# Performance work log

Measured on AMD Instinct MI355X. Metric: run time of the kernel, lower is better.

## Reference

```python
import jax, jax.numpy as jnp
import numpy as np

N, E, B, EP = 100000, 1600000, 512, 200000
NIN, NEMB, HID, NL = 64, 64, 72, 3
EPS = 1e-5


def setup_inputs() -> dict:
    key = jax.random.key(0)
    ks = jax.random.split(key, 20)
    inp = {
        'x': jax.random.normal(ks[0], (N, NIN), jnp.float32),
        'emb': jax.random.normal(ks[1], (N, NEMB), jnp.float32),
        'assign': jax.random.uniform(ks[2], (N, B), jnp.float32),
        'edge_index': jax.random.randint(ks[3], (2, E), 0, N, jnp.int64),
        'pedge_index': jax.random.randint(ks[4], (2, EP), 0, B, jnp.int64),
        # params (xavier-ish scale)
        'node_w': jax.random.normal(ks[5], (NIN, HID), jnp.float32) / np.sqrt(NIN),
        'node_b': jnp.zeros((HID,), jnp.float32),
        'emb_w': jax.random.normal(ks[6], (NEMB, HID), jnp.float32) / np.sqrt(NEMB),
        'emb_b': jnp.zeros((HID,), jnp.float32),
        'conv_winit': jax.random.normal(ks[7], (NL, HID, HID), jnp.float32) / np.sqrt(HID),
        'conv_wroot': jax.random.normal(ks[8], (NL, HID, HID), jnp.float32) / np.sqrt(HID),
        'conv_bias': jnp.zeros((NL, HID), jnp.float32),
        'bn_gamma': jnp.ones((NL, HID), jnp.float32),
        'bn_beta': jnp.zeros((NL, HID), jnp.float32),
        'mlp_w1': jax.random.normal(ks[9], (12 * HID, HID), jnp.float32) / np.sqrt(12 * HID),
        'mlp_b1': jnp.zeros((HID,), jnp.float32),
        'mlp_w2': jax.random.normal(ks[10], (HID, 1), jnp.float32) / np.sqrt(HID),
        'mlp_b2': jnp.zeros((1,), jnp.float32),
    }
    return inp


def _forward(x, emb, assign, node_w, node_b, emb_w, emb_b, conv_winit,
             conv_wroot, conv_bias, bn_gamma, bn_beta, mlp_w1, mlp_b1,
             mlp_w2, mlp_b2, edge_index, pedge_index):
    n = x.shape[0]
    nb = assign.shape[1]
    row, col = edge_index[0], edge_index[1]
    # gcn_norm without self-loops (ARMAConv): D^{-1/2} A D^{-1/2}
    deg = jax.ops.segment_sum(jnp.ones((row.shape[0],), x.dtype), col, num_segments=n)
    dis = jnp.where(deg > 0, jax.lax.rsqrt(jnp.maximum(deg, 1.0)) * jnp.where(deg > 0, 1.0, 0.0), 0.0)
    dis = jnp.where(deg > 0, deg ** -0.5, 0.0)
    norm = dis[row] * dis[col]

    h = jax.nn.relu(x @ node_w + node_b)  # [N, HID]
    for l in range(NL):
        # ARMAConv K=1, T=1: relu(A_hat (h Wi) + h Wr + b)
        m = norm[:, None] * (h @ conv_winit[l])[row]        # [E, HID]
        agg = jax.ops.segment_sum(m, col, num_segments=n)   # [N, HID]
        h = jax.nn.relu(agg + h @ conv_wroot[l] + conv_bias[l])
        # F.relu applied again in forward (idempotent), then BatchNorm (training stats)
        mu = h.mean(0)
        var = ((h - mu) ** 2).mean(0)
        h = (h - mu) * jax.lax.rsqrt(var + EPS) * bn_gamma[l] + bn_beta[l]

    e = jax.nn.relu(emb @ emb_w + emb_b)
    z = jnp.concatenate([h, e], axis=-1)  # [N, 2*HID]

    batch = jnp.argmax(assign, axis=-1)
    cnt = jax.ops.segment_sum(jnp.ones((n,), z.dtype), batch, num_segments=nb)
    p1 = jax.ops.segment_sum(z, batch, num_segments=nb)
    p2 = jax.ops.segment_max(z, batch, num_segments=nb)
    p3 = p1 / jnp.maximum(cnt, 1.0)[:, None]
    xp = jnp.concatenate([p1, p2, p3], axis=-1)  # [B, 6*HID]

    pair = jnp.concatenate([xp[pedge_index[0]], xp[pedge_index[1]]], axis=1)  # [EP, 12*HID]
    out = jnp.tanh(pair @ mlp_w1 + mlp_b1) @ mlp_w2 + mlp_b2
    return out


def reference(x, emb, assign, edge_index, pedge_index, node_w, node_b, emb_w,
              emb_b, conv_winit, conv_wroot, conv_bias, bn_gamma, bn_beta,
              mlp_w1, mlp_b1, mlp_w2, mlp_b2):
    return _forward(x, emb, assign, node_w, node_b, emb_w, emb_b, conv_winit,
                    conv_wroot, conv_bias, bn_gamma, bn_beta, mlp_w1, mlp_b1,
                    mlp_w2, mlp_b2, edge_index, pedge_index)
```

## Files before the change

### kernel.cpp

```cpp
#include <hip/hip_runtime.h>
#include <hip/hip_bf16.h>

#define HID 72
#define EPSV 1e-5f
#define CAP 64
#define DP 76
#define GF 128
#define GA 2048

__device__ __forceinline__ float tanh_fast(float x) {
    float cx = fminf(fmaxf(x, -15.f), 15.f);
    float e = __expf(2.f * cx);
    return __fdividef(e - 1.f, e + 1.f);
}
__device__ __forceinline__ void fma4(float4& a, float w, const float4 v) {
    a.x += w * v.x; a.y += w * v.y; a.z += w * v.z; a.w += w * v.w;
}

__global__ void k_init(int* deg, float* stats, int* bcnt, int N, int statlen, int B) {
    int i = blockIdx.x * blockDim.x + threadIdx.x;
    if (i < N) deg[i] = 0;
    if (i < statlen) stats[i] = 0.f;
    if (i < B) bcnt[i] = 0;
}

__global__ __launch_bounds__(256) void k_front(const int* __restrict__ row, const int* __restrict__ col,
                                               int* __restrict__ deg, int* __restrict__ csr_r, int E,
                                               const float* __restrict__ x, const float* __restrict__ node_w,
                                               const float* __restrict__ node_b, float* __restrict__ t_buf,
                                               const float* __restrict__ emb, const float* __restrict__ emb_w,
                                               const float* __restrict__ emb_b, float* __restrict__ e_buf,
                                               const float* __restrict__ assign, int* __restrict__ batchv,
                                               int* __restrict__ bcnt, int N, int B, int GD) {
    __shared__ float ws[HID][DP];
    int tid = threadIdx.x;
    int bid = blockIdx.x;

    if (bid < GF) {
        int stride = GF * 256 * 8;
        for (int base = (bid * 256 + tid) * 8; base < E; base += stride) {
            #pragma unroll
            for (int h = 0; h < 2; h++) {
                int eb = base + h * 4;
                if (eb + 3 < E) {
                    int4 cc = *(const int4*)(col + eb);
                    int4 rr = *(const int4*)(row + eb);
                    int p0 = atomicAdd(&deg[cc.x], 1);
                    int p1 = atomicAdd(&deg[cc.y], 1);
                    int p2 = atomicAdd(&deg[cc.z], 1);
                    int p3 = atomicAdd(&deg[cc.w], 1);
                    if (p0 < CAP) csr_r[(size_t)cc.x * CAP + p0] = rr.x;
                    if (p1 < CAP) csr_r[(size_t)cc.y * CAP + p1] = rr.y;
                    if (p2 < CAP) csr_r[(size_t)cc.z * CAP + p2] = rr.z;
                    if (p3 < CAP) csr_r[(size_t)cc.w * CAP + p3] = rr.w;
                } else if (eb < E) {
                    int lim = (eb + 4 < E) ? eb + 4 : E;
                    for (int e = eb; e < lim; e++) {
                        int c = col[e];
                        int pos = atomicAdd(&deg[c], 1);
                        if (pos < CAP) csr_r[(size_t)c * CAP + pos] = row[e];
                    }
                }
            }
        }
        return;
    }
    bid -= GF;
    if (bid < 2 * GD) {
        const float* xin; const float* W; const float* bias; float* out;
        int tb = bid;
        if (tb < GD) { xin = x;   W = node_w; bias = node_b; out = t_buf; }
        else         { xin = emb; W = emb_w;  bias = emb_b;  out = e_buf; tb -= GD; }
        int n0 = tb * 128;
        for (int i = tid; i < 64 * HID; i += 256) {
            int k = i / HID, f = i % HID;
            ws[f][k] = W[i];
        }
        __syncthreads();
        int tn = tid & 31;
        int tf = (tid >> 5) * 9;
        float acc[4][9];
        #pragma unroll
        for (int j = 0; j < 9; j++) {
            float b = bias[tf + j];
            acc[0][j] = b; acc[1][j] = b; acc[2][j] = b; acc[3][j] = b;
        }
        int g0 = n0 + tn;
        const float4* xp0 = (const float4*)(xin + (size_t)(g0      < N ? g0      : N - 1) * 64);
        const float4* xp1 = (const float4*)(xin + (size_t)(g0 + 32 < N ? g0 + 32 : N - 1) * 64);
        const float4* xp2 = (const float4*)(xin + (size_t)(g0 + 64 < N ? g0 + 64 : N - 1) * 64);
        const float4* xp3 = (const float4*)(xin + (size_t)(g0 + 96 < N ? g0 + 96 : N - 1) * 64);
        #pragma unroll 2
        for (int k4 = 0; k4 < 16; k4++) {
            float4 h0 = xp0[k4];
            float4 h1 = xp1[k4];
            float4 h2 = xp2[k4];
            float4 h3 = xp3[k4];
            int k = k4 * 4;
            #pragma unroll
            for (int j = 0; j < 9; j++) {
                float4 w = *(const float4*)&ws[tf + j][k];
                acc[0][j] += h0.x * w.x + h0.y * w.y + h0.z * w.z + h0.w * w.w;
                acc[1][j] += h1.x * w.x + h1.y * w.y + h1.z * w.z + h1.w * w.w;
                acc[2][j] += h2.x * w.x + h2.y * w.y + h2.z * w.z + h2.w * w.w;
                acc[3][j] += h3.x * w.x + h3.y * w.y + h3.z * w.z + h3.w * w.w;
            }
        }
        #pragma unroll
        for (int i = 0; i < 4; i++) {
            int gn = n0 + tn + 32 * i;
            if (gn >= N) continue;
            float* dst = out + (size_t)gn * HID + tf;
            #pragma unroll
            for (int j = 0; j < 9; j++) dst[j] = fmaxf(acc[i][j], 0.f);
        }
        return;
    }
    bid -= 2 * GD;
    int wib = tid >> 6;
    int lane = tid & 63;
    int nq = B / 4;
    for (int n = bid * 4 + wib; n < N; n += GA * 4) {
        const float4* rp4 = (const float4*)(assign + (size_t)n * B);
        float best = -INFINITY;
        int bidx = 0x7fffffff;
        for (int q = lane; q < nq; q += 64) {
            float4 v = rp4[q];
            int j = q * 4;
            if (v.x > best) { best = v.x; bidx = j; }
            if (v.y > best) { best = v.y; bidx = j + 1; }
            if (v.z > best) { best = v.z; bidx = j + 2; }
            if (v.w > best) { best = v.w; bidx = j + 3; }
        }
        #pragma unroll
        for (int off = 32; off > 0; off >>= 1) {
            float ov = __shfl_down(best, off);
            int oi = __shfl_down(bidx, off);
            if (ov > best || (ov == best && oi < bidx)) { best = ov; bidx = oi; }
        }
        if (lane == 0) {
            batchv[n] = bidx;
            atomicAdd(&bcnt[bidx], 1);
        }
    }
}

#define CP 76
template <bool BN, bool DIS>
__global__ __launch_bounds__(256) void k_conv_t(const float* t, const float* __restrict__ stats,
                                                const float* __restrict__ gamma, const float* __restrict__ beta,
                                                const float* __restrict__ wi, const float* __restrict__ wr,
                                                const float* __restrict__ cb, float* __restrict__ hw,
                                                float* agg, int N, float invN,
                                                const int* __restrict__ deg, float* __restrict__ dis) {
    __shared__ float hs[64][CP];
    __shared__ float ws[2 * HID][CP];
    int tid = threadIdx.x;
    int n0 = blockIdx.x * 64;
    if constexpr (DIS) {
        if (tid < 64) {
            int gn = n0 + tid;
            if (gn < N) {
                int d = deg[gn];
                dis[gn] = (d > 0) ? rsqrtf((float)d) : 0.f;
            }
        }
    }
    for (int i = tid; i < HID * 2 * HID; i += 256) {
        int k = i / (2 * HID), f = i % (2 * HID);
        ws[f][k] = (f < HID) ? wi[k * HID + f] : wr[k * HID + (f - HID)];
    }
    for (int i = tid; i < 64 * HID; i += 256) {
        int n = i / HID, f = i % HID;
        int gn = n0 + n;
        float v = (gn < N) ? t[(size_t)gn * HID + f] : 0.f;
        if constexpr (BN) {
            float mu = stats[f] * invN;
            float var = stats[HID + f] * invN - mu * mu;
            v = (v - mu) * rsqrtf(var + EPSV) * gamma[f] + beta[f];
        }
        hs[n][f] = v;
    }
    __syncthreads();
    int tn = tid & 15;
    int tf = (tid >> 4) * 9;
    float acc[4][9];
    #pragma unroll
    for (int j = 0; j < 9; j++) {
        float b = (tf >= HID) ? cb[tf - HID + j] : 0.f;
        acc[0][j] = b; acc[1][j] = b; acc[2][j] = b; acc[3][j] = b;
    }
    #pragma unroll 2
    for (int k4 = 0; k4 < HID / 4; k4++) {
        int k = k4 * 4;
        float4 h0 = *(const float4*)&hs[tn][k];
        float4 h1 = *(const float4*)&hs[tn + 16][k];
        float4 h2 = *(const float4*)&hs[tn + 32][k];
        float4 h3 = *(const float4*)&hs[tn + 48][k];
        #pragma unroll
        for (int j = 0; j < 9; j++) {
            float4 w = *(const float4*)&ws[tf + j][k];
            acc[0][j] += h0.x * w.x + h0.y * w.y + h0.z * w.z + h0.w * w.w;
            acc[1][j] += h1.x * w.x + h1.y * w.y + h1.z * w.z + h1.w * w.w;
            acc[2][j] += h2.x * w.x + h2.y * w.y + h2.z * w.z + h2.w * w.w;
            acc[3][j] += h3.x * w.x + h3.y * w.y + h3.z * w.z + h3.w * w.w;
        }
    }
    #pragma unroll
    for (int i = 0; i < 4; i++) {
        int gn = n0 + tn + 16 * i;
        if (gn >= N) continue;
        float* dst = (tf < HID) ? (hw + (size_t)gn * HID + tf) : (agg + (size_t)gn * HID + (tf - HID));
        #pragma unroll
        for (int j = 0; j < 9; j++) dst[j] = acc[i][j];
    }
}

__global__ __launch_bounds__(256) void k_gather9(const float* __restrict__ hw, const int* __restrict__ deg,
                                                 const int* __restrict__ csr_r, const float* __restrict__ dis,
                                                 float* t, int N) {
    int tid = blockIdx.x * blockDim.x + threadIdx.x;
    int n = tid / 9;
    int s = tid - n * 9;
    if (n >= N) return;
    float4* trow = (float4*)(t + (size_t)n * HID) + s * 2;
    float4 a0 = trow[0], a1 = trow[1];
    int d = deg[n];
    d = (d > CAP) ? CAP : d;
    float disc = dis[n];
    const int* crow = csr_r + (size_t)n * CAP;
    const float4* hb = (const float4*)hw + s * 2;
    for (int j0 = 0; j0 < d; j0 += 4) {
        int4 rr = *(const int4*)(crow + j0);
        int rem = d - j0;
        {
            float w = disc * dis[rr.x];
            const float4* hp = hb + (size_t)rr.x * 18;
            fma4(a0, w, hp[0]); fma4(a1, w, hp[1]);
        }
        if (rem > 1) {
            float w = disc * dis[rr.y];
            const float4* hp = hb + (size_t)rr.y * 18;
            fma4(a0, w, hp[0]); fma4(a1, w, hp[1]);
        }
        if (rem > 2) {
            float w = disc * dis[rr.z];
            const float4* hp = hb + (size_t)rr.z * 18;
            fma4(a0, w, hp[0]); fma4(a1, w, hp[1]);
        }
        if (rem > 3) {
            float w = disc * dis[rr.w];
            const float4* hp = hb + (size_t)rr.w * 18;
            fma4(a0, w, hp[0]); fma4(a1, w, hp[1]);
        }
    }
    trow[0] = make_float4(fmaxf(a0.x, 0.f), fmaxf(a0.y, 0.f), fmaxf(a0.z, 0.f), fmaxf(a0.w, 0.f));
    trow[1] = make_float4(fmaxf(a1.x, 0.f), fmaxf(a1.y, 0.f), fmaxf(a1.z, 0.f), fmaxf(a1.w, 0.f));
}

__global__ __launch_bounds__(256) void k_stats(const float* __restrict__ t, float* __restrict__ st, int total4) {
    __shared__ float s1[HID], s2[HID];
    int tx = threadIdx.x;
    if (tx < HID) s1[tx] = 0.f;
    else if (tx < 2 * HID) s2[tx - HID] = 0.f;
    __syncthreads();
    int stride = gridDim.x * blockDim.x;
    int i0 = blockIdx.x * blockDim.x + tx;
    int f0 = (i0 * 4) % HID;
    float a0 = 0, a1 = 0, a2 = 0, a3 = 0, q0 = 0, q1 = 0, q2 = 0, q3 = 0;
    const float4* tp = (const float4*)t;
    for (int i = i0; i < total4; i += stride) {
        float4 v = tp[i];
        a0 += v.x; q0 += v.x * v.x;
        a1 += v.y; q1 += v.y * v.y;
        a2 += v.z; q2 += v.z * v.z;
        a3 += v.w; q3 += v.w * v.w;
    }
    atomicAdd(&s1[f0 + 0], a0); atomicAdd(&s2[f0 + 0], q0);
    atomicAdd(&s1[f0 + 1], a1); atomicAdd(&s2[f0 + 1], q1);
    atomicAdd(&s1[f0 + 2], a2); atomicAdd(&s2[f0 + 2], q2);
    atomicAdd(&s1[f0 + 3], a3); atomicAdd(&s2[f0 + 3], q3);
    __syncthreads();
    if (tx < HID) {
        atomicAdd(&st[tx], s1[tx]);
        atomicAdd(&st[HID + tx], s2[tx]);
    }
}

__global__ __launch_bounds__(1024) void k_bscan(const int* __restrict__ bcnt, int* __restrict__ boffs,
                                                int* __restrict__ bcur, int B) {
    __shared__ int lds[1024];
    int t = threadIdx.x;
    int v = (t < B) ? bcnt[t] : 0;
    lds[t] = v;
    __syncthreads();
    for (int off = 1; off < 1024; off <<= 1) {
        int x = (t >= off) ? lds[t - off] : 0;
        __syncthreads();
        lds[t] += x;
        __syncthreads();
    }
    if (t < B) {
        int excl = lds[t] - v;
        boffs[t] = excl;
        bcur[t] = excl;
    }
}

__global__ void k_bfill(const int* __restrict__ batchv, int* __restrict__ bcur, int* __restrict__ nlist, int N) {
    int n = blockIdx.x * blockDim.x + threadIdx.x;
    if (n < N) {
        int b = batchv[n];
        int pos = atomicAdd(&bcur[b], 1);
        nlist[pos] = n;
    }
}

__global__ __launch_bounds__(576) void k_poolB(const float* __restrict__ t2, const float* __restrict__ ebuf,
                                               const float* __restrict__ stats2, const float* __restrict__ g2,
                                               const float* __restrict__ bt2, const int* __restrict__ boffs,
                                               const int* __restrict__ bcnt, const int* __restrict__ nlist,
                                               float* __restrict__ xp, float invN) {
    __shared__ float ls[4][2 * HID], lm[4][2 * HID];
    int b = blockIdx.x;
    int tid = threadIdx.x;
    int f = tid % (2 * HID);
    int ch = tid / (2 * HID);
    bool isH = f < HID;
    float a = 1.f, sh = 0.f;
    const float* src;
    if (isH) {
        float s1v = stats2[f], s2v = stats2[HID + f];
        float mu = s1v * invN;
        float var = s2v * invN - mu * mu;
        float inv = rsqrtf(var + EPSV);
        a = inv * g2[f];
        sh = bt2[f] - mu * a;
        src = t2 + f;
    } else {
        src = ebuf + (f - HID);
    }
    int s = boffs[b];
    int c = bcnt[b];
    int e = s + c;
    float sum = 0.f, mx = -INFINITY;
    for (int i = s + ch; i < e; i += 4) {
        float v = src[(size_t)nlist[i] * HID] * a + sh;
        sum += v;
        mx = fmaxf(mx, v);
    }
    ls[ch][f] = sum;
    lm[ch][f] = mx;
    __syncthreads();
    if (ch == 0) {
        float stot = ls[0][f] + ls[1][f] + ls[2][f] + ls[3][f];
        float mtot = fmaxf(fmaxf(lm[0][f], lm[1][f]), fmaxf(lm[2][f], lm[3][f]));
        float* xr = xp + (size_t)b * (6 * HID);
        xr[f] = stot;
        xr[2 * HID + f] = mtot;
        xr[4 * HID + f] = stot / fmaxf((float)c, 1.f);
    }
}

__global__ __launch_bounds__(192) void k_uv(const float* __restrict__ xp, const float* __restrict__ w1,
                                            const float* __restrict__ b1, float* __restrict__ U,
                                            float* __restrict__ V) {
    int b = blockIdx.x;
    int t = threadIdx.x;
    if (t >= 2 * HID) return;
    int half = t / HID;
    int f = t % HID;
    const float* xr = xp + (size_t)b * (6 * HID);
    const float* wb = w1 + (size_t)half * (6 * HID) * HID + f;
    float acc = (half == 0) ? b1[f] : 0.f;
    #pragma unroll 4
    for (int k = 0; k < 6 * HID; k++) acc += xr[k] * wb[(size_t)k * HID];
    if (half == 0) U[(size_t)b * HID + f] = acc;
    else           V[(size_t)b * HID + f] = acc;
}

__global__ __launch_bounds__(256) void k_edge(const int* __restrict__ pe, const float* __restrict__ U,
                                              const float* __restrict__ V, const float* __restrict__ w2,
                                              const float* __restrict__ b2, float* __restrict__ out, int EP) {
    int ep = blockIdx.x * blockDim.x + threadIdx.x;
    if (ep >= EP) return;
    int a = pe[ep];
    int b = pe[EP + ep];
    const float4* up = (const float4*)(U + (size_t)a * HID);
    const float4* vp = (const float4*)(V + (size_t)b * HID);
    float s = 0.f;
    #pragma unroll
    for (int q = 0; q < HID / 4; q++) {
        float4 u = up[q];
        float4 v = vp[q];
        s += tanh_fast(u.x + v.x) * w2[q * 4 + 0];
        s += tanh_fast(u.y + v.y) * w2[q * 4 + 1];
        s += tanh_fast(u.z + v.z) * w2[q * 4 + 2];
        s += tanh_fast(u.w + v.w) * w2[q * 4 + 3];
    }
    out[ep] = s + b2[0];
}

extern "C" void kernel_launch(void* const* d_in, const int* in_sizes, int n_in,
                              void* d_out, int out_size, void* d_ws, size_t ws_size,
                              hipStream_t stream) {
    const float* x       = (const float*)d_in[0];
    const float* emb     = (const float*)d_in[1];
    const float* assign  = (const float*)d_in[2];
    const int*   ei      = (const int*)d_in[3];
    const int*   pe      = (const int*)d_in[4];
    const float* node_w  = (const float*)d_in[5];
    const float* node_b  = (const float*)d_in[6];
    const float* emb_w   = (const float*)d_in[7];
    const float* emb_b   = (const float*)d_in[8];
    const float* conv_wi = (const float*)d_in[9];
    const float* conv_wr = (const float*)d_in[10];
    const float* conv_b  = (const float*)d_in[11];
    const float* bn_g    = (const float*)d_in[12];
    const float* bn_b    = (const float*)d_in[13];
    const float* w1      = (const float*)d_in[14];
    const float* b1      = (const float*)d_in[15];
    const float* w2      = (const float*)d_in[16];
    const float* b2      = (const float*)d_in[17];

    int N = in_sizes[0] / 64;
    int B = in_sizes[2] / N;
    int E = in_sizes[3] / 2;
    int EP = in_sizes[4] / 2;
    float invN = 1.0f / (float)N;

    char* wp = (char*)d_ws;
    auto alloc = [&](size_t nbytes) -> void* {
        void* p = (void*)wp;
        wp += (nbytes + 255) & ~(size_t)255;
        return p;
    };
    float* t_buf  = (float*)alloc((size_t)N * HID * 4);
    float* hw     = (float*)alloc((size_t)N * HID * 4);
    float* e_buf  = (float*)alloc((size_t)N * HID * 4);
    int*   csr_r  = (int*)alloc((size_t)N * CAP * 4);
    int*   deg    = (int*)alloc((size_t)N * 4);
    float* dis    = (float*)alloc((size_t)N * 4);
    int*   batchv = (int*)alloc((size_t)N * 4);
    int*   nlist  = (int*)alloc((size_t)N * 4);
    float* stats  = (float*)alloc((size_t)3 * 2 * HID * 4);
    int*   bcnt   = (int*)alloc((size_t)B * 4);
    int*   boffs  = (int*)alloc((size_t)B * 4);
    int*   bcur   = (int*)alloc((size_t)B * 4);
    float* xp     = (float*)alloc((size_t)B * 6 * HID * 4);
    float* Ub     = (float*)alloc((size_t)B * HID * 4);
    float* Vb     = (float*)alloc((size_t)B * HID * 4);

    const int* row = ei;
    const int* col = ei + E;

    int nb256_N = (N + 255) / 256;
    int GD = (N + 127) / 128;

    k_init<<<nb256_N, 256, 0, stream>>>(deg, stats, bcnt, N, 3 * 2 * HID, B);

    k_front<<<GF + 2 * GD + GA, 256, 0, stream>>>(row, col, deg, csr_r, E,
                                                  x, node_w, node_b, t_buf,
                                                  emb, emb_w, emb_b, e_buf,
                                                  assign, batchv, bcnt, N, B, GD);

    for (int l = 0; l < 3; l++) {
        const float* wi = conv_wi + (size_t)l * HID * HID;
        const float* wr = conv_wr + (size_t)l * HID * HID;
        const float* cb = conv_b + (size_t)l * HID;
        if (l == 0)
            k_conv_t<false, true><<<(N + 63) / 64, 256, 0, stream>>>(t_buf, nullptr, nullptr, nullptr,
                                                                     wi, wr, cb, hw, t_buf, N, invN,
                                                                     deg, dis);
        else
            k_conv_t<true, false><<<(N + 63) / 64, 256, 0, stream>>>(t_buf, stats + (size_t)(l - 1) * 2 * HID,
                                                                     bn_g + (size_t)(l - 1) * HID,
                                                                     bn_b + (size_t)(l - 1) * HID,
                                                                     wi, wr, cb, hw, t_buf, N, invN,
                                                                     nullptr, nullptr);
        k_gather9<<<(9 * N + 255) / 256, 256, 0, stream>>>(hw, deg, csr_r, dis, t_buf, N);
        k_stats<<<288, 256, 0, stream>>>(t_buf, stats + (size_t)l * 2 * HID, N * HID / 4);
    }

    k_bscan<<<1, 1024, 0, stream>>>(bcnt, boffs, bcur, B);
    k_bfill<<<nb256_N, 256, 0, stream>>>(batchv, bcur, nlist, N);
    k_poolB<<<B, 576, 0, stream>>>(t_buf, e_buf, stats + (size_t)2 * 2 * HID,
                                   bn_g + (size_t)2 * HID, bn_b + (size_t)2 * HID,
                                   boffs, bcnt, nlist, xp, invN);
    k_uv<<<B, 192, 0, stream>>>(xp, w1, b1, Ub, Vb);
    k_edge<<<(EP + 255) / 256, 256, 0, stream>>>(pe, Ub, Vb, w2, b2, (float*)d_out, EP);
}
```

Before: 1.235 ms.

## Fuse init, node GEMM, layer-0 conv, and batch scan/fill into fewer launches

Result: no change. 1.227 ms (-0.6%).

```diff
diff --git a/kernel.cpp b/kernel.cpp
--- a/kernel.cpp
+++ b/kernel.cpp
@@ -5,7 +5,7 @@
 #define EPSV 1e-5f
 #define CAP 64
 #define DP 76
-#define GF 128
+#define GF 384
 #define GA 2048
 
 __device__ __forceinline__ float tanh_fast(float x) {
@@ -16,23 +16,79 @@
 __device__ __forceinline__ void fma4(float4& a, float w, const float4 v) {
     a.x += w * v.x; a.y += w * v.y; a.z += w * v.z; a.w += w * v.w;
 }
-
-__global__ void k_init(int* deg, float* stats, int* bcnt, int N, int statlen, int B) {
-    int i = blockIdx.x * blockDim.x + threadIdx.x;
-    if (i < N) deg[i] = 0;
-    if (i < statlen) stats[i] = 0.f;
-    if (i < B) bcnt[i] = 0;
-}
-
-__global__ __launch_bounds__(256) void k_front(const int* __restrict__ row, const int* __restrict__ col,
-                                               int* __restrict__ deg, int* __restrict__ csr_r, int E,
-                                               const float* __restrict__ x, const float* __restrict__ node_w,
-                                               const float* __restrict__ node_b, float* __restrict__ t_buf,
-                                               const float* __restrict__ emb, const float* __restrict__ emb_w,
-                                               const float* __restrict__ emb_b, float* __restrict__ e_buf,
-                                               const float* __restrict__ assign, int* __restrict__ batchv,
-                                               int* __restrict__ bcnt, int N, int B, int GD) {
+__device__ __forceinline__ float inv_sqrt_deg(int d) {
+    return (d > 0) ? rsqrtf((float)d) : 0.f;
+}
+
+__global__ __launch_bounds__(256) void k_d1(const float* __restrict__ x, const float* __restrict__ node_w,
+                                            const float* __restrict__ node_b, float* __restrict__ t_buf,
+                                            int* __restrict__ deg, float* __restrict__ stats,
+                                            int* __restrict__ bcnt, int N, int B, int GD) {
     __shared__ float ws[HID][DP];
+    int tid = threadIdx.x;
+    int bid = blockIdx.x;
+    if (bid >= GD) {
+        int j = (bid - GD) * 256 + tid;
+        if (j < N) deg[j] = 0;
+        if (j < 3 * 2 * HID) stats[j] = 0.f;
+        if (j < B) bcnt[j] = 0;
+        return;
+    }
+    int n0 = bid * 128;
+    for (int i = tid; i < 64 * HID; i += 256) {
+        int k = i / HID, f = i % HID;
+        ws[f][k] = node_w[i];
+    }
+    __syncthreads();
+    int tn = tid & 31;
+    int tf = (tid >> 5) * 9;
+    float acc[4][9];
+    #pragma unroll
+    for (int j = 0; j < 9; j++) {
+        float b = node_b[tf + j];
+        acc[0][j] = b; acc[1][j] = b; acc[2][j] = b; acc[3][j] = b;
+    }
+    int g0 = n0 + tn;
+    const float4* xp0 = (const float4*)(x + (size_t)(g0      < N ? g0      : N - 1) * 64);
+    const float4* xp1 = (const float4*)(x + (size_t)(g0 + 32 < N ? g0 + 32 : N - 1) * 64);
+    const float4* xp2 = (const float4*)(x + (size_t)(g0 + 64 < N ? g0 + 64 : N - 1) * 64);
+    const float4* xp3 = (const float4*)(x + (size_t)(g0 + 96 < N ? g0 + 96 : N - 1) * 64);
+    #pragma unroll 2
+    for (int k4 = 0; k4 < 16; k4++) {
+        float4 h0 = xp0[k4];
+        float4 h1 = xp1[k4];
+        float4 h2 = xp2[k4];
+        float4 h3 = xp3[k4];
+        int k = k4 * 4;
+        #pragma unroll
+        for (int j = 0; j < 9; j++) {
+            float4 w = *(const float4*)&ws[tf + j][k];
+            acc[0][j] += h0.x * w.x + h0.y * w.y + h0.z * w.z + h0.w * w.w;
+            acc[1][j] += h1.x * w.x + h1.y * w.y + h1.z * w.z + h1.w * w.w;
+            acc[2][j] += h2.x * w.x + h2.y * w.y + h2.z * w.z + h2.w * w.w;
+            acc[3][j] += h3.x * w.x + h3.y * w.y + h3.z * w.z + h3.w * w.w;
+        }
+    }
+    #pragma unroll
+    for (int i = 0; i < 4; i++) {
+        int gn = n0 + tn + 32 * i;
+        if (gn >= N) continue;
+        float* dst = t_buf + (size_t)gn * HID + tf;
+        #pragma unroll
+        for (int j = 0; j < 9; j++) dst[j] = fmaxf(acc[i][j], 0.f);
+    }
+}
+
+__global__ __launch_bounds__(256) void k_front2(const int* __restrict__ row, const int* __restrict__ col,
+                                                int* __restrict__ deg, int* __restrict__ csr_r, int E,
+                                                const float* __restrict__ wi0, const float* __restrict__ wr0,
+                                                const float* __restrict__ cb0, float* __restrict__ t_buf,
+                                                float* __restrict__ hw,
+                                                const float* __restrict__ emb, const float* __restrict__ emb_w,
+                                                const float* __restrict__ emb_b, float* __restrict__ e_buf,
+                                                const float* __restrict__ assign, int* __restrict__ batchv,
+                                                int* __restrict__ bcnt, int N, int B, int GDE, int GC) {
+    __shared__ float ws2[2 * HID][DP];
     int tid = threadIdx.x;
     int bid = blockIdx.x;
 
@@ -66,15 +122,59 @@
         return;
     }
     bid -= GF;
-    if (bid < 2 * GD) {
-        const float* xin; const float* W; const float* bias; float* out;
-        int tb = bid;
-        if (tb < GD) { xin = x;   W = node_w; bias = node_b; out = t_buf; }
-        else         { xin = emb; W = emb_w;  bias = emb_b;  out = e_buf; tb -= GD; }
-        int n0 = tb * 128;
+    if (bid < GC) {
+        int n0 = bid * 64;
+        for (int i = tid; i < HID * 2 * HID; i += 256) {
+            int k = i / (2 * HID), f = i % (2 * HID);
+            ws2[f][k] = (f < HID) ? wi0[k * HID + f] : wr0[k * HID + (f - HID)];
+        }
+        __syncthreads();
+        int tn = tid & 15;
+        int tf = (tid >> 4) * 9;
+        float acc[4][9];
+        #pragma unroll
+        for (int j = 0; j < 9; j++) {
+            float b = (tf >= HID) ? cb0[tf - HID + j] : 0.f;
+            acc[0][j] = b; acc[1][j] = b; acc[2][j] = b; acc[3][j] = b;
+        }
+        int g0 = n0 + tn;
+        const float* r0 = t_buf + (size_t)(g0      < N ? g0      : N - 1) * HID;
+        const float* r1 = t_buf + (size_t)(g0 + 16 < N ? g0 + 16 : N - 1) * HID;
+        const float* r2 = t_buf + (size_t)(g0 + 32 < N ? g0 + 32 : N - 1) * HID;
+        const float* r3 = t_buf + (size_t)(g0 + 48 < N ? g0 + 48 : N - 1) * HID;
+        #pragma unroll 2
+        for (int k4 = 0; k4 < HID / 4; k4++) {
+            int k = k4 * 4;
+            float4 h0 = *(const float4*)(r0 + k);
+            float4 h1 = *(const float4*)(r1 + k);
+            float4 h2 = *(const float4*)(r2 + k);
+            float4 h3 = *(const float4*)(r3 + k);
+            #pragma unroll
+            for (int j = 0; j < 9; j++) {
+                float4 w = *(const float4*)&ws2[tf + j][k];
+                acc[0][j] += h0.x * w.x + h0.y * w.y + h0.z * w.z + h0.w * w.w;
+                acc[1][j] += h1.x * w.x + h1.y * w.y + h1.z * w.z + h1.w * w.w;
+                acc[2][j] += h2.x * w.x + h2.y * w.y + h2.z * w.z + h2.w * w.w;
+                acc[3][j] += h3.x * w.x + h3.y * w.y + h3.z * w.z + h3.w * w.w;
+            }
+        }
+        __syncthreads();
+        #pragma unroll
+        for (int i = 0; i < 4; i++) {
+            int gn = n0 + tn + 16 * i;
+            if (gn >= N) continue;
+            float* dst = (tf < HID) ? (hw + (size_t)gn * HID + tf) : (t_buf + (size_t)gn * HID + (tf - HID));
+            #pragma unroll
+            for (int j = 0; j < 9; j++) dst[j] = acc[i][j];
+        }
+        return;
+    }
+    bid -= GC;
+    if (bid < GDE) {
+        int n0 = bid * 128;
         for (int i = tid; i < 64 * HID; i += 256) {
             int k = i / HID, f = i % HID;
-            ws[f][k] = W[i];
+            ws2[f][k] = emb_w[i];
         }
         __syncthreads();
         int tn = tid & 31;
@@ -82,14 +182,14 @@
         float acc[4][9];
         #pragma unroll
         for (int j = 0; j < 9; j++) {
-            float b = bias[tf + j];
+            float b = emb_b[tf + j];
             acc[0][j] = b; acc[1][j] = b; acc[2][j] = b; acc[3][j] = b;
         }
         int g0 = n0 + tn;
-        const float4* xp0 = (const float4*)(xin + (size_t)(g0      < N ? g0      : N - 1) * 64);
-        const float4* xp1 = (const float4*)(xin + (size_t)(g0 + 32 < N ? g0 + 32 : N - 1) * 64);
-        const float4* xp2 = (const float4*)(xin + (size_t)(g0 + 64 < N ? g0 + 64 : N - 1) * 64);
-        const float4* xp3 = (const float4*)(xin + (size_t)(g0 + 96 < N ? g0 + 96 : N - 1) * 64);
+        const float4* xp0 = (const float4*)(emb + (size_t)(g0      < N ? g0      : N - 1) * 64);
+        const float4* xp1 = (const float4*)(emb + (size_t)(g0 + 32 < N ? g0 + 32 : N - 1) * 64);
+        const float4* xp2 = (const float4*)(emb + (size_t)(g0 + 64 < N ? g0 + 64 : N - 1) * 64);
+        const float4* xp3 = (const float4*)(emb + (size_t)(g0 + 96 < N ? g0 + 96 : N - 1) * 64);
         #pragma unroll 2
         for (int k4 = 0; k4 < 16; k4++) {
             float4 h0 = xp0[k4];
@@ -99,7 +199,7 @@
             int k = k4 * 4;
             #pragma unroll
             for (int j = 0; j < 9; j++) {
-                float4 w = *(const float4*)&ws[tf + j][k];
+                float4 w = *(const float4*)&ws2[tf + j][k];
                 acc[0][j] += h0.x * w.x + h0.y * w.y + h0.z * w.z + h0.w * w.w;
                 acc[1][j] += h1.x * w.x + h1.y * w.y + h1.z * w.z + h1.w * w.w;
                 acc[2][j] += h2.x * w.x + h2.y * w.y + h2.z * w.z + h2.w * w.w;
@@ -110,13 +210,13 @@
         for (int i = 0; i < 4; i++) {
             int gn = n0 + tn + 32 * i;
             if (gn >= N) continue;
-            float* dst = out + (size_t)gn * HID + tf;
+            float* dst = e_buf + (size_t)gn * HID + tf;
             #pragma unroll
             for (int j = 0; j < 9; j++) dst[j] = fmaxf(acc[i][j], 0.f);
         }
         return;
     }
-    bid -= 2 * GD;
+    bid -= GDE;
     int wib = tid >> 6;
     int lane = tid & 63;
     int nq = B / 4;
@@ -145,27 +245,101 @@
     }
 }
 
+__global__ __launch_bounds__(256) void k_gather9(const float* __restrict__ hw, const int* __restrict__ deg,
+                                                 const int* __restrict__ csr_r, float* t, int N,
+                                                 int scanB, const int* __restrict__ bcnt,
+                                                 int* __restrict__ boffs, int* __restrict__ bcur) {
+    if (scanB && blockIdx.x == gridDim.x - 1) {
+        int lane = threadIdx.x;
+        if (lane < 64) {
+            int c[8];
+            int tot = 0;
+            int base = lane * 8;
+            #pragma unroll
+            for (int j = 0; j < 8; j++) {
+                int idx = base + j;
+                c[j] = (idx < scanB) ? bcnt[idx] : 0;
+                tot += c[j];
+            }
+            int v = tot;
+            #pragma unroll
+            for (int off = 1; off < 64; off <<= 1) {
+                int u = __shfl_up(v, off);
+                if (lane >= off) v += u;
+            }
+            int run = v - tot;
+            #pragma unroll
+            for (int j = 0; j < 8; j++) {
+                int idx = base + j;
+                if (idx < scanB) {
+                    boffs[idx] = run;
+                    bcur[idx] = run;
+                    run += c[j];
+                }
+            }
+        }
+        return;
+    }
+    int tid = blockIdx.x * blockDim.x + threadIdx.x;
+    int n = tid / 9;
+    int s = tid - n * 9;
+    if (n >= N) return;
+    float4* trow = (float4*)(t + (size_t)n * HID) + s * 2;
+    float4 a0 = trow[0], a1 = trow[1];
+    int dn = deg[n];
+    int d = (dn > CAP) ? CAP : dn;
+    float disc = inv_sqrt_deg(dn);
+    const int* crow = csr_r + (size_t)n * CAP;
+    const float4* hb = (const float4*)hw + s * 2;
+    for (int j0 = 0; j0 < d; j0 += 4) {
+        int4 rr = *(const int4*)(crow + j0);
+        int rem = d - j0;
+        {
+            float w = disc * inv_sqrt_deg(deg[rr.x]);
+            const float4* hp = hb + (size_t)rr.x * 18;
+            fma4(a0, w, hp[0]); fma4(a1, w, hp[1]);
+        }
+        if (rem > 1) {
+            float w = disc * inv_sqrt_deg(deg[rr.y]);
+            const float4* hp = hb + (size_t)rr.y * 18;
+            fma4(a0, w, hp[0]); fma4(a1, w, hp[1]);
+        }
+        if (rem > 2) {
+            float w = disc * inv_sqrt_deg(deg[rr.z]);
+            const float4* hp = hb + (size_t)rr.z * 18;
+            fma4(a0, w, hp[0]); fma4(a1, w, hp[1]);
+        }
+        if (rem > 3) {
+            float w = disc * inv_sqrt_deg(deg[rr.w]);
+            const float4* hp = hb + (size_t)rr.w * 18;
+            fma4(a0, w, hp[0]); fma4(a1, w, hp[1]);
+        }
+    }
+    trow[0] = make_float4(fmaxf(a0.x, 0.f), fmaxf(a0.y, 0.f), fmaxf(a0.z, 0.f), fmaxf(a0.w, 0.f));
+    trow[1] = make_float4(fmaxf(a1.x, 0.f), fmaxf(a1.y, 0.f), fmaxf(a1.z, 0.f), fmaxf(a1.w, 0.f));
+}
+
 #define CP 76
-template <bool BN, bool DIS>
 __global__ __launch_bounds__(256) void k_conv_t(const float* t, const float* __restrict__ stats,
                                                 const float* __restrict__ gamma, const float* __restrict__ beta,
                                                 const float* __restrict__ wi, const float* __restrict__ wr,
                                                 const float* __restrict__ cb, float* __restrict__ hw,
-                                                float* agg, int N, float invN,
-                                                const int* __restrict__ deg, float* __restrict__ dis) {
+                                                float* agg, int N, float invN, int gcBlocks,
+                                                const int* __restrict__ batchv, int* __restrict__ bcur,
+                                                int* __restrict__ nlist) {
     __shared__ float hs[64][CP];
     __shared__ float ws[2 * HID][CP];
     int tid = threadIdx.x;
+    if ((int)blockIdx.x >= gcBlocks) {
+        int n = ((int)blockIdx.x - gcBlocks) * 256 + tid;
+        if (n < N) {
+            int b = batchv[n];
+            int pos = atomicAdd(&bcur[b], 1);
+            nlist[pos] = n;
+        }
+        return;
+    }
     int n0 = blockIdx.x * 64;
-    if constexpr (DIS) {
-        if (tid < 64) {
-            int gn = n0 + tid;
-            if (gn < N) {
-                int d = deg[gn];
-                dis[gn] = (d > 0) ? rsqrtf((float)d) : 0.f;
-            }
-        }
-    }
     for (int i = tid; i < HID * 2 * HID; i += 256) {
         int k = i / (2 * HID), f = i % (2 * HID);
         ws[f][k] = (f < HID) ? wi[k * HID + f] : wr[k * HID + (f - HID)];
@@ -174,11 +348,9 @@
         int n = i / HID, f = i % HID;
         int gn = n0 + n;
         float v = (gn < N) ? t[(size_t)gn * HID + f] : 0.f;
-        if constexpr (BN) {
-            float mu = stats[f] * invN;
-            float var = stats[HID + f] * invN - mu * mu;
-            v = (v - mu) * rsqrtf(var + EPSV) * gamma[f] + beta[f];
-        }
+        float mu = stats[f] * invN;
+        float var = stats[HID + f] * invN - mu * mu;
+        v = (v - mu) * rsqrtf(var + EPSV) * gamma[f] + beta[f];
         hs[n][f] = v;
     }
     __syncthreads();
@@ -214,48 +386,6 @@
         #pragma unroll
         for (int j = 0; j < 9; j++) dst[j] = acc[i][j];
     }
-}
-
-__global__ __launch_bounds__(256) void k_gather9(const float* __restrict__ hw, const int* __restrict__ deg,
-                                                 const int* __restrict__ csr_r, const float* __restrict__ dis,
-                                                 float* t, int N) {
-    int tid = blockIdx.x * blockDim.x + threadIdx.x;
-    int n = tid / 9;
-    int s = tid - n * 9;
-    if (n >= N) return;
-    float4* trow = (float4*)(t + (size_t)n * HID) + s * 2;
-    float4 a0 = trow[0], a1 = trow[1];
-    int d = deg[n];
-    d = (d > CAP) ? CAP : d;
-    float disc = dis[n];
-    const int* crow = csr_r + (size_t)n * CAP;
-    const float4* hb = (const float4*)hw + s * 2;
-    for (int j0 = 0; j0 < d; j0 += 4) {
-        int4 rr = *(const int4*)(crow + j0);
-        int rem = d - j0;
-        {
-            float w = disc * dis[rr.x];
-            const float4* hp = hb + (size_t)rr.x * 18;
-            fma4(a0, w, hp[0]); fma4(a1, w, hp[1]);
-        }
-        if (rem > 1) {
-            float w = disc * dis[rr.y];
-            const float4* hp = hb + (size_t)rr.y * 18;
-            fma4(a0, w, hp[0]); fma4(a1, w, hp[1]);
-        }
-        if (rem > 2) {
-            float w = disc * dis[rr.z];
-            const float4* hp = hb + (size_t)rr.z * 18;
-            fma4(a0, w, hp[0]); fma4(a1, w, hp[1]);
-        }
-        if (rem > 3) {
-            float w = disc * dis[rr.w];
-            const float4* hp = hb + (size_t)rr.w * 18;
-            fma4(a0, w, hp[0]); fma4(a1, w, hp[1]);
-        }
-    }
-    trow[0] = make_float4(fmaxf(a0.x, 0.f), fmaxf(a0.y, 0.f), fmaxf(a0.z, 0.f), fmaxf(a0.w, 0.f));
-    trow[1] = make_float4(fmaxf(a1.x, 0.f), fmaxf(a1.y, 0.f), fmaxf(a1.z, 0.f), fmaxf(a1.w, 0.f));
 }
 
 __global__ __launch_bounds__(256) void k_stats(const float* __restrict__ t, float* __restrict__ st, int total4) {
@@ -284,35 +414,6 @@
     if (tx < HID) {
         atomicAdd(&st[tx], s1[tx]);
         atomicAdd(&st[HID + tx], s2[tx]);
-    }
-}
-
-__global__ __launch_bounds__(1024) void k_bscan(const int* __restrict__ bcnt, int* __restrict__ boffs,
-                                                int* __restrict__ bcur, int B) {
-    __shared__ int lds[1024];
-    int t = threadIdx.x;
-    int v = (t < B) ? bcnt[t] : 0;
-    lds[t] = v;
-    __syncthreads();
-    for (int off = 1; off < 1024; off <<= 1) {
-        int x = (t >= off) ? lds[t - off] : 0;
-        __syncthreads();
-        lds[t] += x;
-        __syncthreads();
-    }
-    if (t < B) {
-        int excl = lds[t] - v;
-        boffs[t] = excl;
-        bcur[t] = excl;
-    }
-}
-
-__global__ void k_bfill(const int* __restrict__ batchv, int* __restrict__ bcur, int* __restrict__ nlist, int N) {
-    int n = blockIdx.x * blockDim.x + threadIdx.x;
-    if (n < N) {
-        int b = batchv[n];
-        int pos = atomicAdd(&bcur[b], 1);
-        nlist[pos] = n;
     }
 }
 
@@ -440,7 +541,6 @@
     float* e_buf  = (float*)alloc((size_t)N * HID * 4);
     int*   csr_r  = (int*)alloc((size_t)N * CAP * 4);
     int*   deg    = (int*)alloc((size_t)N * 4);
-    float* dis    = (float*)alloc((size_t)N * 4);
     int*   batchv = (int*)alloc((size_t)N * 4);
     int*   nlist  = (int*)alloc((size_t)N * 4);
     float* stats  = (float*)alloc((size_t)3 * 2 * HID * 4);
@@ -454,38 +554,35 @@
     const int* row = ei;
     const int* col = ei + E;
 
-    int nb256_N = (N + 255) / 256;
     int GD = (N + 127) / 128;
-
-    k_init<<<nb256_N, 256, 0, stream>>>(deg, stats, bcnt, N, 3 * 2 * HID, B);
-
-    k_front<<<GF + 2 * GD + GA, 256, 0, stream>>>(row, col, deg, csr_r, E,
-                                                  x, node_w, node_b, t_buf,
-                                                  emb, emb_w, emb_b, e_buf,
-                                                  assign, batchv, bcnt, N, B, GD);
-
-    for (int l = 0; l < 3; l++) {
-        const float* wi = conv_wi + (size_t)l * HID * HID;
-        const float* wr = conv_wr + (size_t)l * HID * HID;
-        const float* cb = conv_b + (size_t)l * HID;
-        if (l == 0)
-            k_conv_t<false, true><<<(N + 63) / 64, 256, 0, stream>>>(t_buf, nullptr, nullptr, nullptr,
-                                                                     wi, wr, cb, hw, t_buf, N, invN,
-                                                                     deg, dis);
-        else
-            k_conv_t<true, false><<<(N + 63) / 64, 256, 0, stream>>>(t_buf, stats + (size_t)(l - 1) * 2 * HID,
-                                                                     bn_g + (size_t)(l - 1) * HID,
-                                                                     bn_b + (size_t)(l - 1) * HID,
-                                                                     wi, wr, cb, hw, t_buf, N, invN,
-                                                                     nullptr, nullptr);
-        k_gather9<<<(9 * N + 255) / 256, 256, 0, stream>>>(hw, deg, csr_r, dis, t_buf, N);
-        k_stats<<<288, 256, 0, stream>>>(t_buf, stats + (size_t)l * 2 * HID, N * HID / 4);
-    }
-
-    k_bscan<<<1, 1024, 0, stream>>>(bcnt, boffs, bcur, B);
-    k_bfill<<<nb256_N, 256, 0, stream>>>(batchv, bcur, nlist, N);
-    k_poolB<<<B, 576, 0, stream>>>(t_buf, e_buf, stats + (size_t)2 * 2 * HID,
-                                   bn_g + (size_t)2 * HID, bn_b + (size_t)2 * HID,
+    int GC = (N + 63) / 64;
+    int GZ = (N + 255) / 256;
+    int GG = (9 * N + 255) / 256;
+
+    k_d1<<<GD + GZ, 256, 0, stream>>>(x, node_w, node_b, t_buf, deg, stats, bcnt, N, B, GD);
+
+    k_front2<<<GF + GC + GD + GA, 256, 0, stream>>>(row, col, deg, csr_r, E,
+                                                    conv_wi, conv_wr, conv_b, t_buf, hw,
+                                                    emb, emb_w, emb_b, e_buf,
+                                                    assign, batchv, bcnt, N, B, GD, GC);
+
+    k_gather9<<<GG + 1, 256, 0, stream>>>(hw, deg, csr_r, t_buf, N, B, bcnt, boffs, bcur);
+    k_stats<<<288, 256, 0, stream>>>(t_buf, stats, N * HID / 4);
+
+    k_conv_t<<<GC + GZ, 256, 0, stream>>>(t_buf, stats, bn_g, bn_b,
+                                          conv_wi + (size_t)HID * HID, conv_wr + (size_t)HID * HID,
+                                          conv_b + HID, hw, t_buf, N, invN, GC, batchv, bcur, nlist);
+    k_gather9<<<GG, 256, 0, stream>>>(hw, deg, csr_r, t_buf, N, 0, nullptr, nullptr, nullptr);
+    k_stats<<<288, 256, 0, stream>>>(t_buf, stats + 2 * HID, N * HID / 4);
+
+    k_conv_t<<<GC, 256, 0, stream>>>(t_buf, stats + 2 * HID, bn_g + HID, bn_b + HID,
+                                     conv_wi + (size_t)2 * HID * HID, conv_wr + (size_t)2 * HID * HID,
+                                     conv_b + 2 * HID, hw, t_buf, N, invN, GC, nullptr, nullptr, nullptr);
+    k_gather9<<<GG, 256, 0, stream>>>(hw, deg, csr_r, t_buf, N, 0, nullptr, nullptr, nullptr);
+    k_stats<<<288, 256, 0, stream>>>(t_buf, stats + 4 * HID, N * HID / 4);
+
+    k_poolB<<<B, 576, 0, stream>>>(t_buf, e_buf, stats + 4 * HID,
+                                   bn_g + 2 * HID, bn_b + 2 * HID,
                                    boffs, bcnt, nlist, xp, invN);
     k_uv<<<B, 192, 0, stream>>>(xp, w1, b1, Ub, Vb);
     k_edge<<<(EP + 255) / 256, 256, 0, stream>>>(pe, Ub, Vb, w2, b2, (float*)d_out, EP);
```
